# Optimization experiments

Measured on AMD Instinct MI355X. Metric: run time of the kernel, lower is better.

Reference implementation:

```python
import jax, jax.numpy as jnp
import numpy as np

B, K, C = 1024, 8, 10   # predicted points, concepts, classes per concept
N = 8192                # background (training) set size
EPS = 1e-13


def setup_inputs() -> dict:
    key = jax.random.key(0)
    k1, k2, k3 = jax.random.split(key, 3)
    c_p = jax.random.normal(k1, (B, K, C), dtype=jnp.float32)
    bandwidth = jnp.ones((K * C,), dtype=jnp.float32)  # learned param, init 1.0
    c_in = jax.random.randint(k2, (N, K), 0, C, dtype=jnp.int64)
    delta_in = jax.random.randint(k3, (N,), 0, 2, dtype=jnp.int32)
    return {"c_p": c_p, "bandwidth": bandwidth, "c_in": c_in, "delta_in": delta_in}


def _beran(c_p, bandwidth, c_in, delta_in):
    # ---- GaussKernel l2 metric ----
    proba = jax.nn.softmax(c_p, axis=-1)                      # [B,K,C]
    bw = jnp.clip(bandwidth, 0.001, 10.0).reshape(K, C)       # [K,C]
    onehot = jax.nn.one_hot(c_in, C, dtype=proba.dtype)       # [N,K,C]
    # sum((p - l)^2 / bw) = sum(p^2/bw) - 2 sum(p*l/bw) + sum(l^2/bw)
    A = jnp.sum(proba * proba / bw, axis=(1, 2))              # [B]
    D = jnp.einsum('nkc,kc->n', onehot, 1.0 / bw)             # [N]
    cross = jnp.einsum('bkc,nkc->bn', proba / bw, onehot)     # [B,N]
    metric = A[:, None] - 2.0 * cross + D[None, :]            # [B,N]
    weights = jnp.exp(-metric)
    s = jnp.sum(weights, axis=1, keepdims=True)               # normalize over background axis
    bad = s < EPS
    W = jnp.where(bad, 0.0, weights / jnp.where(bad, 1.0, s)) # [B,N]

    # ---- Beran cumulative hazard scan ----
    w_cumsum = jnp.cumsum(W, axis=1)
    shifted = w_cumsum - W
    ones = jnp.ones_like(shifted)
    bad2 = jnp.isclose(shifted, ones) | jnp.isclose(w_cumsum, ones)
    shifted = jnp.where(bad2, 0.0, shifted)
    w_cumsum = jnp.where(bad2, 0.0, w_cumsum)
    xi = jnp.log(1.0 - shifted) - jnp.log(1.0 - w_cumsum)
    filtered_xi = delta_in.astype(xi.dtype)[None, :] * xi
    hazards = jnp.cumsum(filtered_xi, axis=1)
    surv_func = jnp.exp(-hazards)                             # [B,N]
    first_step = 1.0 - surv_func[:, :1]
    surv_steps = jnp.concatenate([first_step, surv_func[:, :-1] - surv_func[:, 1:]], axis=1)
    ss = jnp.sum(surv_steps, axis=1, keepdims=True)
    bad3 = ss < EPS
    surv_steps = jnp.where(bad3, 0.0, surv_steps / jnp.where(bad3, 1.0, ss))
    return surv_func, surv_steps


def reference(c_p, bandwidth, c_in, delta_in):
    return _beran(c_p, bandwidth, c_in, delta_in)
```

## Files before the change

### kernel.cpp

```cpp
#include <hip/hip_runtime.h>

#define NN 8192
#define BB 1024
#define KK 8
#define CC 10
#define NT 1024
#define CHUNK (NN/NT)
#define NW (NT/64)
#define T3SZ 2100

__global__ void pack_kernel(const int* __restrict__ c_in, const int* __restrict__ delta_in,
                            unsigned* __restrict__ pairs, unsigned* __restrict__ dmask_g) {
    int n = blockIdx.x * blockDim.x + threadIdx.x;
    if (n >= NN) return;
    const int4* p = reinterpret_cast<const int4*>(c_in + (size_t)n * KK);
    int4 lo = p[0], hi = p[1];
    unsigned g0 = (unsigned)((lo.x * 10 + lo.y) * 10 + lo.z);
    unsigned g1 = (unsigned)((lo.w * 10 + hi.x) * 10 + hi.y);
    unsigned g2 = (unsigned)(hi.z * 10 + hi.w);
    pairs[n] = g0 | (g1 << 10) | (g2 << 20);
    unsigned long long bal = __ballot(delta_in[n] & 1);
    if ((threadIdx.x & 63) == 0) {
        dmask_g[n >> 5]       = (unsigned)(bal & 0xffffffffull);
        dmask_g[(n >> 5) + 1] = (unsigned)(bal >> 32);
    }
}

__global__ __launch_bounds__(NT, 8) void beran_kernel(
    const float* __restrict__ c_p, const float* __restrict__ bandwidth,
    const int* __restrict__ c_in, const int* __restrict__ delta_in,
    const unsigned* __restrict__ pairs, const unsigned* __restrict__ dmask_g,
    float* __restrict__ out)
{
    __shared__ float tb[KK * CC];
    __shared__ float Apart[KK];
    __shared__ float t3[T3SZ];
    __shared__ float wsA[NW];
    __shared__ float wsM[NW];

    const int b    = blockIdx.x;
    const int t    = threadIdx.x;
    const int lane = t & 63;
    const int wv   = t >> 6;
    const int base = t * CHUNK;

    if (t < KK) {
        const int k = t;
        float v[CC];
        float mx = -1e30f;
        #pragma unroll
        for (int c = 0; c < CC; c++) { v[c] = c_p[((size_t)b*KK + k)*CC + c]; mx = fmaxf(mx, v[c]); }
        float se = 0.0f;
        #pragma unroll
        for (int c = 0; c < CC; c++) { v[c] = __expf(v[c] - mx); se += v[c]; }
        float inv = 1.0f / se;
        float Ak = 0.0f;
        #pragma unroll
        for (int c = 0; c < CC; c++) {
            float p  = v[c] * inv;
            float bw = bandwidth[k*CC + c];
            bw = fminf(fmaxf(bw, 0.001f), 10.0f);
            float ib = 1.0f / bw;
            tb[k*CC + c] = ib - 2.0f * p * ib;
            Ak += p * p * ib;
        }
        Apart[k] = Ak;
    }
    __syncthreads();

    for (int i = t; i < T3SZ; i += NT) {
        float v;
        if (i < 1000) {
            v = tb[0*CC + i/100] + tb[1*CC + (i/10)%10] + tb[2*CC + i%10];
        } else if (i < 2000) {
            int j = i - 1000;
            v = tb[3*CC + j/100] + tb[4*CC + (j/10)%10] + tb[5*CC + j%10];
        } else {
            int q = i - 2000;
            float Ar = 0.0f;
            #pragma unroll
            for (int k = 0; k < KK; k++) Ar += Apart[k];
            v = tb[6*CC + q/10] + tb[7*CC + q%10] + Ar;
        }
        t3[i] = -v;
    }
    __syncthreads();

    float creg[CHUNK];
    unsigned dm = 0;
    float run = 0.0f;
    if (pairs) {
        dm = (dmask_g[t >> 2] >> ((t & 3) * 8)) & 0xffu;
        uint4 v0 = *reinterpret_cast<const uint4*>(pairs + base);
        uint4 v1 = *reinterpret_cast<const uint4*>(pairs + base + 4);
        unsigned pk[CHUNK] = {v0.x, v0.y, v0.z, v0.w, v1.x, v1.y, v1.z, v1.w};
        #pragma unroll
        for (int i = 0; i < CHUNK; i++) {
            unsigned w0 = pk[i];
            float m = t3[w0 & 1023] + t3[1000 + ((w0 >> 10) & 1023)]
                    + t3[2000 + (w0 >> 20)];
            run += __expf(m);
            creg[i] = run;
        }
    } else {
        float A = 0.0f;
        #pragma unroll
        for (int k = 0; k < KK; k++) A += Apart[k];
        #pragma unroll
        for (int i = 0; i < CHUNK; i++) {
            const int4* p4 = reinterpret_cast<const int4*>(c_in + (size_t)(base + i) * KK);
            int4 lo = p4[0], hi = p4[1];
            float m = A;
            m += tb[0*CC + lo.x] + tb[1*CC + lo.y] + tb[2*CC + lo.z] + tb[3*CC + lo.w];
            m += tb[4*CC + hi.x] + tb[5*CC + hi.y] + tb[6*CC + hi.z] + tb[7*CC + hi.w];
            run += __expf(-m);
            creg[i] = run;
            dm |= (unsigned)(delta_in[base + i] & 1) << i;
        }
    }

    float x = run;
    #pragma unroll
    for (int d = 1; d < 64; d <<= 1) {
        float y = __shfl_up(x, d);
        if (lane >= d) x += y;
    }
    if (lane == 63) wsA[wv] = x;
    __syncthreads();
    float excl = __shfl_up(x, 1);
    if (lane == 0) excl = 0.0f;
    float s = 0.0f, woff = 0.0f;
    #pragma unroll
    for (int w = 0; w < NW; w++) {
        float y = wsA[w];
        s += y;
        if (w < wv) woff += y;
    }
    const float off_raw = woff + excl;
    const float invs = (s < 1e-13f) ? 0.0f : 1.0f / s;

    const float ISO = 1.00001e-5f;
    float uprev = 1.0f - off_raw * invs;
    float P = 1.0f;
    #pragma unroll
    for (int i = 0; i < CHUNK; i++) {
        float cs = (creg[i] + off_raw) * invs;
        float u  = 1.0f - cs;
        bool bad  = (fabsf(uprev) <= ISO) || (fabsf(u) <= ISO);
        bool flag = (dm >> i) & 1u;
        float f = (flag && !bad) ? u * __builtin_amdgcn_rcpf(uprev) : 1.0f;
        P *= f;
        creg[i] = P;
        uprev = u;
    }

    float xm = P;
    #pragma unroll
    for (int d = 1; d < 64; d <<= 1) {
        float y = __shfl_up(xm, d);
        if (lane >= d) xm *= y;
    }
    if (lane == 63) wsM[wv] = xm;
    __syncthreads();
    float exclm = __shfl_up(xm, 1);
    if (lane == 0) exclm = 1.0f;
    float tot = 1.0f, moff = 1.0f;
    #pragma unroll
    for (int w = 0; w < NW; w++) {
        float y = wsM[w];
        tot *= y;
        if (w < wv) moff *= y;
    }
    const float S_base = moff * exclm;
    const float surv_last = tot;
    const float ss = 1.0f - surv_last;
    const float invss = (ss < 1e-13f) ? 0.0f : 1.0f / ss;

    #pragma unroll
    for (int i = 0; i < CHUNK; i++) creg[i] = S_base * creg[i];

    const float wave_base = __shfl(S_base, 0);
    const float g1sp     = __shfl(creg[7], 31);

    float* outS = out + (size_t)b * NN;
    float* outT = out + (size_t)BB * NN + (size_t)b * NN;
    const bool hi = (lane & 1);
    #pragma unroll
    for (int g = 0; g < 2; g++) {
        const int o = 32 * g + (lane >> 1);
        float e0 = __shfl(creg[0], o), e1 = __shfl(creg[1], o);
        float e2 = __shfl(creg[2], o), e3 = __shfl(creg[3], o);
        float o0 = __shfl(creg[4], o), o1 = __shfl(creg[5], o);
        float o2 = __shfl(creg[6], o), o3 = __shfl(creg[7], o);
        float s0 = hi ? o0 : e0, s1 = hi ? o1 : e1;
        float s2 = hi ? o2 : e2, s3 = hi ? o3 : e3;
        float sp = __shfl_up(s3, 1);
        if (lane == 0) sp = (g == 0) ? wave_base : g1sp;
        const int n0 = wv * 512 + g * 256 + lane * 4;
        *reinterpret_cast<float4*>(outS + n0) = make_float4(s0, s1, s2, s3);
        *reinterpret_cast<float4*>(outT + n0) =
            make_float4((sp - s0) * invss, (s0 - s1) * invss,
                        (s1 - s2) * invss, (s2 - s3) * invss);
    }
}

extern "C" void kernel_launch(void* const* d_in, const int* in_sizes, int n_in,
                              void* d_out, int out_size, void* d_ws, size_t ws_size,
                              hipStream_t stream) {
    const float* c_p       = (const float*)d_in[0];
    const float* bandwidth = (const float*)d_in[1];
    const int*   c_in      = (const int*)d_in[2];
    const int*   delta_in  = (const int*)d_in[3];
    float* out = (float*)d_out;

    unsigned* pairs   = nullptr;
    unsigned* dmask_g = nullptr;
    const size_t need = (size_t)NN * sizeof(unsigned) + (size_t)(NN / 32) * sizeof(unsigned);
    if (ws_size >= need) {
        pairs   = (unsigned*)d_ws;
        dmask_g = (unsigned*)((char*)d_ws + (size_t)NN * sizeof(unsigned));
        pack_kernel<<<NN / 256, 256, 0, stream>>>(c_in, delta_in, pairs, dmask_g);
    }
    beran_kernel<<<BB, NT, 0, stream>>>(c_p, bandwidth, c_in, delta_in, pairs, dmask_g, out);
}
```

Baseline: 32.71 us.

## Halve block size and stage output transpose through swizzled LDS

```diff
diff --git a/kernel.cpp b/kernel.cpp
--- a/kernel.cpp
+++ b/kernel.cpp
@@ -4,10 +4,15 @@
 #define BB 1024
 #define KK 8
 #define CC 10
-#define NT 1024
+#define NT 512
 #define CHUNK (NN/NT)
 #define NW (NT/64)
 #define T3SZ 2100
+#define HALF 4096
+
+__device__ __forceinline__ int swz(int n) {
+    return (n & ~31) | ((n + (n >> 5)) & 31);
+}
 
 __global__ void pack_kernel(const int* __restrict__ c_in, const int* __restrict__ delta_in,
                             unsigned* __restrict__ pairs, unsigned* __restrict__ dmask_g) {
@@ -32,11 +37,13 @@
     const unsigned* __restrict__ pairs, const unsigned* __restrict__ dmask_g,
     float* __restrict__ out)
 {
+    __shared__ float a2[HALF];
     __shared__ float tb[KK * CC];
     __shared__ float Apart[KK];
     __shared__ float t3[T3SZ];
     __shared__ float wsA[NW];
     __shared__ float wsM[NW];
+    __shared__ float s4095;
 
     const int b    = blockIdx.x;
     const int t    = threadIdx.x;
@@ -90,17 +97,19 @@
     unsigned dm = 0;
     float run = 0.0f;
     if (pairs) {
-        dm = (dmask_g[t >> 2] >> ((t & 3) * 8)) & 0xffu;
-        uint4 v0 = *reinterpret_cast<const uint4*>(pairs + base);
-        uint4 v1 = *reinterpret_cast<const uint4*>(pairs + base + 4);
-        unsigned pk[CHUNK] = {v0.x, v0.y, v0.z, v0.w, v1.x, v1.y, v1.z, v1.w};
-        #pragma unroll
-        for (int i = 0; i < CHUNK; i++) {
-            unsigned w0 = pk[i];
-            float m = t3[w0 & 1023] + t3[1000 + ((w0 >> 10) & 1023)]
-                    + t3[2000 + (w0 >> 20)];
-            run += __expf(m);
-            creg[i] = run;
+        dm = (dmask_g[t >> 1] >> ((t & 1) * 16)) & 0xffffu;
+        #pragma unroll
+        for (int g = 0; g < CHUNK / 4; g++) {
+            uint4 v = *reinterpret_cast<const uint4*>(pairs + base + g * 4);
+#define DO3(w0, idx) { \
+            float m = t3[(w0) & 1023] + t3[1000 + (((w0) >> 10) & 1023)] \
+                    + t3[2000 + ((w0) >> 20)]; \
+            run += __expf(m); creg[idx] = run; }
+            DO3(v.x, g*4 + 0)
+            DO3(v.y, g*4 + 1)
+            DO3(v.z, g*4 + 2)
+            DO3(v.w, g*4 + 3)
+#undef DO3
         }
     } else {
         float A = 0.0f;
@@ -127,8 +136,6 @@
     }
     if (lane == 63) wsA[wv] = x;
     __syncthreads();
-    float excl = __shfl_up(x, 1);
-    if (lane == 0) excl = 0.0f;
     float s = 0.0f, woff = 0.0f;
     #pragma unroll
     for (int w = 0; w < NW; w++) {
@@ -136,7 +143,7 @@
         s += y;
         if (w < wv) woff += y;
     }
-    const float off_raw = woff + excl;
+    const float off_raw = woff + (x - run);
     const float invs = (s < 1e-13f) ? 0.0f : 1.0f / s;
 
     const float ISO = 1.00001e-5f;
@@ -162,8 +169,6 @@
     }
     if (lane == 63) wsM[wv] = xm;
     __syncthreads();
-    float exclm = __shfl_up(xm, 1);
-    if (lane == 0) exclm = 1.0f;
     float tot = 1.0f, moff = 1.0f;
     #pragma unroll
     for (int w = 0; w < NW; w++) {
@@ -171,36 +176,42 @@
         tot *= y;
         if (w < wv) moff *= y;
     }
+    float exclm = __shfl_up(xm, 1);
+    if (lane == 0) exclm = 1.0f;
     const float S_base = moff * exclm;
-    const float surv_last = tot;
-    const float ss = 1.0f - surv_last;
+
+    #pragma unroll
+    for (int i = 0; i < CHUNK; i++) creg[i] = S_base * creg[i];
+    if (t == NT/2) s4095 = S_base;
+
+    const float ss = 1.0f - tot;
     const float invss = (ss < 1e-13f) ? 0.0f : 1.0f / ss;
-
-    #pragma unroll
-    for (int i = 0; i < CHUNK; i++) creg[i] = S_base * creg[i];
-
-    const float wave_base = __shfl(S_base, 0);
-    const float g1sp     = __shfl(creg[7], 31);
-
     float* outS = out + (size_t)b * NN;
     float* outT = out + (size_t)BB * NN + (size_t)b * NN;
-    const bool hi = (lane & 1);
-    #pragma unroll
-    for (int g = 0; g < 2; g++) {
-        const int o = 32 * g + (lane >> 1);
-        float e0 = __shfl(creg[0], o), e1 = __shfl(creg[1], o);
-        float e2 = __shfl(creg[2], o), e3 = __shfl(creg[3], o);
-        float o0 = __shfl(creg[4], o), o1 = __shfl(creg[5], o);
-        float o2 = __shfl(creg[6], o), o3 = __shfl(creg[7], o);
-        float s0 = hi ? o0 : e0, s1 = hi ? o1 : e1;
-        float s2 = hi ? o2 : e2, s3 = hi ? o3 : e3;
-        float sp = __shfl_up(s3, 1);
-        if (lane == 0) sp = (g == 0) ? wave_base : g1sp;
-        const int n0 = wv * 512 + g * 256 + lane * 4;
-        *reinterpret_cast<float4*>(outS + n0) = make_float4(s0, s1, s2, s3);
-        *reinterpret_cast<float4*>(outT + n0) =
-            make_float4((sp - s0) * invss, (s0 - s1) * invss,
-                        (s1 - s2) * invss, (s2 - s3) * invss);
+
+    #pragma unroll
+    for (int sidx = 0; sidx < 2; sidx++) {
+        __syncthreads();
+        if ((t >> 8) == sidx) {
+            const int lb = base - sidx * HALF;
+            #pragma unroll
+            for (int i = 0; i < CHUNK; i++) a2[swz(lb + i)] = creg[i];
+        }
+        __syncthreads();
+        #pragma unroll
+        for (int j = 0; j < 2; j++) {
+            const int nl = j * 2048 + t * 4;
+            const int n0 = sidx * HALF + nl;
+            float s0 = a2[swz(nl)];
+            float s1 = a2[swz(nl + 1)];
+            float s2 = a2[swz(nl + 2)];
+            float s3 = a2[swz(nl + 3)];
+            float sp = (nl == 0) ? ((sidx == 0) ? 1.0f : s4095) : a2[swz(nl - 1)];
+            *reinterpret_cast<float4*>(outS + n0) = make_float4(s0, s1, s2, s3);
+            *reinterpret_cast<float4*>(outT + n0) =
+                make_float4((sp - s0) * invss, (s0 - s1) * invss,
+                            (s1 - s2) * invss, (s2 - s3) * invss);
+        }
     }
 }
 
```

Measured after the change: 28.05 us. 1.17x faster.
